# Kernel optimization log

Measured on AMD Instinct MI355X. Metric: run time of the kernel, lower is better.

The kernel has to match this reference:

```python
import jax, jax.numpy as jnp
import numpy as np

EPS = 1e-5

def layer_norm(x, gamma, beta):
    m = jnp.mean(x, axis=-1, keepdims=True)
    v = jnp.var(x, axis=-1, keepdims=True)
    return (x - m) / jnp.sqrt(v + EPS) * gamma + beta


def setup_inputs() -> dict:
    key = jax.random.key(0)
    ks = jax.random.split(key, 10)
    B, N, D = 2, 2048, 1024
    H, Dh = 16, 64
    C, CD = 256, 512
    inner = H * Dh  # 1024
    J = C + 1 + N  # 2305 = context + null + self

    x = jax.random.normal(ks[0], (B, N, D), dtype=jnp.float32)
    context = jax.random.normal(ks[1], (B, C, CD), dtype=jnp.float32)
    mask = jax.random.uniform(ks[2], (B, C + N)) < 0.9  # bool, mostly True
    attn_bias = jax.random.normal(ks[3], (H, N, J), dtype=jnp.float32) * 0.02

    norm_gamma = jnp.ones((D,), dtype=jnp.float32)
    null_kv = jax.random.normal(ks[4], (2, Dh), dtype=jnp.float32)
    Wq = jax.random.normal(ks[5], (D, inner), dtype=jnp.float32) * (D ** -0.5)
    Wkv = jax.random.normal(ks[6], (D, 2 * Dh), dtype=jnp.float32) * (D ** -0.5)
    ctx_ln_w = jnp.ones((CD,), dtype=jnp.float32)
    ctx_ln_b = jnp.zeros((CD,), dtype=jnp.float32)
    Wctx = jax.random.normal(ks[7], (CD, 2 * Dh), dtype=jnp.float32) * (CD ** -0.5)
    bctx = jnp.zeros((2 * Dh,), dtype=jnp.float32)
    Wout = jax.random.normal(ks[8], (inner, D), dtype=jnp.float32) * (inner ** -0.5)
    out_gamma = jnp.ones((D,), dtype=jnp.float32)

    return {"x": x, "context": context, "mask": mask, "attn_bias": attn_bias,
            "norm_gamma": norm_gamma, "null_kv": null_kv, "Wq": Wq, "Wkv": Wkv,
            "ctx_ln_w": ctx_ln_w, "ctx_ln_b": ctx_ln_b, "Wctx": Wctx, "bctx": bctx,
            "Wout": Wout, "out_gamma": out_gamma}


def reference(x, context, mask, attn_bias, norm_gamma, null_kv, Wq, Wkv,
              ctx_ln_w, ctx_ln_b, Wctx, bctx, Wout, out_gamma):
    B, N, D = x.shape
    Dh = null_kv.shape[-1]
    H = Wq.shape[-1] // Dh
    scale = Dh ** -0.5

    xn = layer_norm(x, norm_gamma, 0.0)
    q = (xn @ Wq).reshape(B, N, H, Dh).transpose(0, 2, 1, 3) * scale  # b h n d
    k, v = jnp.split(xn @ Wkv, 2, axis=-1)  # b n d each (multi-query: shared across heads)

    # prepend learned null kv token
    nk = jnp.broadcast_to(null_kv[0], (B, 1, Dh))
    nv = jnp.broadcast_to(null_kv[1], (B, 1, Dh))
    k = jnp.concatenate([nk, k], axis=1)
    v = jnp.concatenate([nv, v], axis=1)

    # prepend projected context tokens
    cn = layer_norm(context, ctx_ln_w, ctx_ln_b)
    ck, cv = jnp.split(cn @ Wctx + bctx, 2, axis=-1)
    k = jnp.concatenate([ck, k], axis=1)  # b j d, j = C + 1 + N
    v = jnp.concatenate([cv, v], axis=1)

    sim = jnp.einsum('bhid,bjd->bhij', q, k) + attn_bias
    # pad mask with True for the null token (left), then broadcast over h, i
    m = jnp.pad(mask, ((0, 0), (1, 0)), constant_values=True)[:, None, None, :]
    max_neg = -jnp.finfo(sim.dtype).max
    sim = jnp.where(m, sim, max_neg)

    attn = jax.nn.softmax(sim.astype(jnp.float32), axis=-1)
    out = jnp.einsum('bhij,bjd->bhid', attn, v)  # b h n d
    out = out.transpose(0, 2, 1, 3).reshape(B, N, H * Dh)
    return layer_norm(out @ Wout, out_gamma, 0.0)
```

## Files before the change

### kernel.cpp

```cpp
#include <hip/hip_runtime.h>

constexpr int B  = 2;
constexpr int N  = 2048;
constexpr int H  = 16;
constexpr int C  = 256;
constexpr int J  = C + 1 + N;
constexpr int Jp = 2368;
constexpr int NT = Jp / 64;
constexpr float EPS = 1e-5f;
constexpr float LOG2E = 1.4426950408889634f;

typedef __bf16 bf16x8 __attribute__((ext_vector_type(8)));
typedef float  f32x4  __attribute__((ext_vector_type(4)));
typedef float  f32x16 __attribute__((ext_vector_type(16)));
typedef unsigned int uint4v __attribute__((ext_vector_type(4)));
typedef __attribute__((address_space(3))) unsigned int lds_u32;
typedef const __attribute__((address_space(1))) unsigned int glb_u32;

__device__ inline void load_lds16(const void* g, void* l) {
    __builtin_amdgcn_global_load_lds((glb_u32*)g, (lds_u32*)l, 16, 0, 0);
}
__device__ inline unsigned short f2bf(float f) {
    unsigned int u = __builtin_bit_cast(unsigned int, f);
    u += 0x7fffu + ((u >> 16) & 1u);
    return (unsigned short)(u >> 16);
}
__device__ inline unsigned int packbf2(float a, float b) {
    union { __bf16 h[2]; unsigned int u; } cv;
    cv.h[0] = (__bf16)a;
    cv.h[1] = (__bf16)b;
    return cv.u;
}
__device__ inline float fexp2(float x) {
    float r;
    asm("v_exp_f32 %0, %1" : "=v"(r) : "v"(x));
    return r;
}
__device__ inline f32x4 mfma16(bf16x8 a, bf16x8 b, f32x4 c) {
    return __builtin_amdgcn_mfma_f32_16x16x32_bf16(a, b, c, 0, 0, 0);
}
__device__ inline f32x16 mfma32(bf16x8 a, bf16x8 b, f32x16 c) {
    return __builtin_amdgcn_mfma_f32_32x32x16_bf16(a, b, c, 0, 0, 0);
}
__device__ inline f32x4 loadu4(const float* p) {
    f32x4 r;
    __builtin_memcpy(&r, p, 16);
    return r;
}

__global__ void mask_prep(const void* __restrict__ mraw, float* __restrict__ maskf) {
    __shared__ int bad_int, bad_f32;
    const int t = threadIdx.x;
    if (t == 0) { bad_int = 0; bad_f32 = 0; }
    __syncthreads();
    const unsigned int* w = (const unsigned int*)mraw;
    int li = 0, lf = 0;
    for (int i = t; i < 1152; i += 256) {
        unsigned int v = w[i];
        if (v > 1u) li = 1;
        if (v != 0u && v != 0x3F800000u) lf = 1;
    }
    if (li) atomicOr(&bad_int, 1);
    if (lf) atomicOr(&bad_f32, 1);
    __syncthreads();
    const int mode = (!bad_int) ? 0 : ((!bad_f32) ? 1 : 2);
    const unsigned char* bytes = (const unsigned char*)mraw;
    for (int i = t; i < 2 * Jp; i += 256) {
        const int b2 = i / Jp, jp = i - b2 * Jp;
        float v;
        if (jp == 0) v = 0.f;
        else if (jp >= J) v = -1e30f;
        else {
            const int idx = b2 * (C + N) + jp - 1;
            const int keep = (mode == 2) ? (bytes[idx] != 0) : (w[idx] != 0u);
            v = keep ? 0.f : -1e30f;
        }
        maskf[i] = v;
    }
}

__global__ void zero_pads(unsigned short* __restrict__ Kb, unsigned short* __restrict__ Vt) {
    const int t = threadIdx.x;
    for (int i = t; i < 2 * 63 * 64; i += 256) {
        const int b2 = i / (63 * 64);
        const int rr = (i / 64) % 63;
        const int d  = i % 64;
        Kb[(size_t)(b2 * Jp + J + rr) * 64 + d] = 0;
    }
    for (int i = t; i < 2 * 64 * 63; i += 256) {
        const int b2 = i / (64 * 63);
        const int d  = (i / 63) % 64;
        const int cc = i % 63;
        Vt[(size_t)(b2 * 64 + d) * Jp + J + cc] = 0;
    }
}

template <int BF16OUT>
__global__ void __launch_bounds__(256) ln1024(const float* __restrict__ x,
                                              const float* __restrict__ gamma,
                                              void* __restrict__ outp) {
    const int row = blockIdx.x;
    const int t = threadIdx.x;
    const float* xr = x + (size_t)row * 1024;
    float4 v = ((const float4*)xr)[t];
    float s  = v.x + v.y + v.z + v.w;
    float ss = v.x * v.x + v.y * v.y + v.z * v.z + v.w * v.w;
    #pragma unroll
    for (int o = 1; o < 64; o <<= 1) {
        s  += __shfl_xor(s, o);
        ss += __shfl_xor(ss, o);
    }
    __shared__ float red[8];
    const int w = t >> 6;
    if ((t & 63) == 0) { red[w * 2] = s; red[w * 2 + 1] = ss; }
    __syncthreads();
    s  = red[0] + red[2] + red[4] + red[6];
    ss = red[1] + red[3] + red[5] + red[7];
    const float mean = s * (1.0f / 1024.0f);
    const float var  = ss * (1.0f / 1024.0f) - mean * mean;
    const float rstd = rsqrtf(var + EPS);
    const float4 g = ((const float4*)gamma)[t];
    float o0 = (v.x - mean) * rstd * g.x;
    float o1 = (v.y - mean) * rstd * g.y;
    float o2 = (v.z - mean) * rstd * g.z;
    float o3 = (v.w - mean) * rstd * g.w;
    if (BF16OUT) {
        ushort4 u;
        u.x = f2bf(o0); u.y = f2bf(o1); u.z = f2bf(o2); u.w = f2bf(o3);
        *(ushort4*)((unsigned short*)outp + (size_t)row * 1024 + t * 4) = u;
    } else {
        *(float4*)((float*)outp + (size_t)row * 1024 + t * 4) = make_float4(o0, o1, o2, o3);
    }
}

__global__ void __launch_bounds__(256) transpose_w(const float* __restrict__ W,
                                                   unsigned short* __restrict__ WT,
                                                   int K, int Nn, float scale) {
    __shared__ float lds[64][68];
    const int k0 = blockIdx.x * 64, n0 = blockIdx.y * 64;
    const int t = threadIdx.x;
    const int kk = t >> 4, nn = (t & 15) * 4;
    #pragma unroll
    for (int r = 0; r < 4; r++) {
        const float4 v = *(const float4*)(W + (size_t)(k0 + kk + r * 16) * Nn + n0 + nn);
        lds[kk + r * 16][nn + 0] = v.x;
        lds[kk + r * 16][nn + 1] = v.y;
        lds[kk + r * 16][nn + 2] = v.z;
        lds[kk + r * 16][nn + 3] = v.w;
    }
    __syncthreads();
    const int nr = t >> 2, kc = (t & 3) * 16;
    #pragma unroll
    for (int u4 = 0; u4 < 4; u4++) {
        ushort4 u;
        u.x = f2bf(lds[kc + u4 * 4 + 0][nr] * scale);
        u.y = f2bf(lds[kc + u4 * 4 + 1][nr] * scale);
        u.z = f2bf(lds[kc + u4 * 4 + 2][nr] * scale);
        u.w = f2bf(lds[kc + u4 * 4 + 3][nr] * scale);
        *(ushort4*)(WT + (size_t)(n0 + nr) * K + k0 + kc + u4 * 4) = u;
    }
}

__global__ void __launch_bounds__(128) ctx_proj(const float* __restrict__ ctx,
                                                const float* __restrict__ lw,
                                                const float* __restrict__ lb,
                                                const float* __restrict__ Wc,
                                                const float* __restrict__ bc,
                                                unsigned short* __restrict__ Kb,
                                                unsigned short* __restrict__ Vt) {
    const int row = blockIdx.x;
    const int b2 = row >> 8, ci = row & 255;
    const int t = threadIdx.x;
    __shared__ float cn[512];
    __shared__ float red[4];
    const float* xr = ctx + (size_t)row * 512;
    float4 v = ((const float4*)xr)[t];
    float s  = v.x + v.y + v.z + v.w;
    float ss = v.x * v.x + v.y * v.y + v.z * v.z + v.w * v.w;
    #pragma unroll
    for (int o = 1; o < 64; o <<= 1) {
        s  += __shfl_xor(s, o);
        ss += __shfl_xor(ss, o);
    }
    const int w = t >> 6;
    if ((t & 63) == 0) { red[w * 2] = s; red[w * 2 + 1] = ss; }
    __syncthreads();
    s  = red[0] + red[2];
    ss = red[1] + red[3];
    const float mean = s * (1.0f / 512.0f);
    const float var  = ss * (1.0f / 512.0f) - mean * mean;
    const float rstd = rsqrtf(var + EPS);
    const float4 g  = ((const float4*)lw)[t];
    const float4 be = ((const float4*)lb)[t];
    float4 c4;
    c4.x = (v.x - mean) * rstd * g.x + be.x;
    c4.y = (v.y - mean) * rstd * g.y + be.y;
    c4.z = (v.z - mean) * rstd * g.z + be.z;
    c4.w = (v.w - mean) * rstd * g.w + be.w;
    *(float4*)&cn[t * 4] = c4;
    __syncthreads();
    float acc = bc[t];
    #pragma unroll 8
    for (int d = 0; d < 512; d++) acc = fmaf(cn[d], Wc[d * 128 + t], acc);
    const unsigned short bv = f2bf(acc);
    if (t < 64) Kb[(size_t)(b2 * Jp + ci) * 64 + t] = bv;
    else        Vt[(size_t)(b2 * 64 + (t - 64)) * Jp + ci] = bv;
}

__global__ void null_fill(const float* __restrict__ nkv,
                          unsigned short* __restrict__ Kb, unsigned short* __restrict__ Vt) {
    const int b2 = blockIdx.x;
    const int t = threadIdx.x;
    Kb[(size_t)(b2 * Jp + 256) * 64 + t] = f2bf(nkv[t]);
    Vt[(size_t)(b2 * 64 + t) * Jp + 256] = f2bf(nkv[64 + t]);
}

template <int MODE>
__global__ void __launch_bounds__(256, 2) gemm_bf16(
        const unsigned short* __restrict__ A, const unsigned short* __restrict__ BT,
        float* __restrict__ Cf, unsigned short* __restrict__ Cb,
        unsigned short* __restrict__ Kb, unsigned short* __restrict__ Vt,
        int M, int Nn, int K) {
    __shared__ __align__(16) unsigned char smem[65536];
    const int t = threadIdx.x;
    const int w = t >> 6, lane = t & 63;
    const int g = lane >> 4, ln15 = lane & 15;
    const int wm = w >> 1, wn = w & 1;
    const int row0 = blockIdx.x * 128, col0 = blockIdx.y * 128;
    const int nk = K >> 6;
    const int ls = lane >> 3;
    const int swz = (lane & 7) ^ ls;

    f32x4 acc[4][4];
    #pragma unroll
    for (int i = 0; i < 4; i++)
        #pragma unroll
        for (int jj = 0; jj < 4; jj++)
            acc[i][jj] = (f32x4){0.f, 0.f, 0.f, 0.f};

    auto stage = [&](int kt, int cur) {
        if (w < 2) {
            const unsigned short* src = A + (size_t)(row0 + w * 64 + ls) * K + kt * 64 + swz * 8;
            unsigned char* dst = smem + cur * 16384 + w * 8192;
            #pragma unroll
            for (int i = 0; i < 8; i++)
                load_lds16(src + (size_t)i * 8 * K, dst + i * 1024);
        } else {
            const unsigned short* src = BT + (size_t)(col0 + (w - 2) * 64 + ls) * K + kt * 64 + swz * 8;
            unsigned char* dst = smem + 32768 + cur * 16384 + (w - 2) * 8192;
            #pragma unroll
            for (int i = 0; i < 8; i++)
                load_lds16(src + (size_t)i * 8 * K, dst + i * 1024);
        }
    };

    stage(0, 0);
    __syncthreads();
    for (int kt = 0; kt < nk; kt++) {
        const int cur = kt & 1;
        if (kt + 1 < nk) stage(kt + 1, cur ^ 1);
        const unsigned char* As = smem + cur * 16384;
        const unsigned char* Bs = smem + 32768 + cur * 16384;
        #pragma unroll
        for (int ks = 0; ks < 2; ks++) {
            bf16x8 af[4], bf[4];
            #pragma unroll
            for (int mq = 0; mq < 4; mq++)
                af[mq] = *(const bf16x8*)(As + (wm * 64 + mq * 16 + ln15) * 128 +
                                          ((ks * 64 + g * 16) ^ ((ln15 & 7) << 4)));
            #pragma unroll
            for (int nq = 0; nq < 4; nq++)
                bf[nq] = *(const bf16x8*)(Bs + (wn * 64 + nq * 16 + ln15) * 128 +
                                          ((ks * 64 + g * 16) ^ ((ln15 & 7) << 4)));
            #pragma unroll
            for (int mq = 0; mq < 4; mq++)
                #pragma unroll
                for (int nq = 0; nq < 4; nq++)
                    acc[mq][nq] = mfma16(af[mq], bf[nq], acc[mq][nq]);
        }
        __syncthreads();
    }

    #pragma unroll
    for (int mq = 0; mq < 4; mq++) {
        #pragma unroll
        for (int nq = 0; nq < 4; nq++) {
            #pragma unroll
            for (int r = 0; r < 4; r++) {
                const int gr = row0 + wm * 64 + mq * 16 + g * 4 + r;
                const int gc = col0 + wn * 64 + nq * 16 + ln15;
                if (MODE == 0) {
                    Cf[(size_t)gr * Nn + gc] = acc[mq][nq][r];
                } else if (MODE == 1) {
                    Cb[(size_t)gr * Nn + gc] = f2bf(acc[mq][nq][r]);
                } else {
                    const int b2 = gr >> 11, tok = gr & 2047;
                    const unsigned short v = f2bf(acc[mq][nq][r]);
                    if (gc < 64) Kb[(size_t)(b2 * Jp + 257 + tok) * 64 + gc] = v;
                    else         Vt[(size_t)(b2 * 64 + gc - 64) * Jp + 257 + tok] = v;
                }
            }
        }
    }
}

__global__ void __launch_bounds__(512, 2) attn_v11(
        const unsigned short* __restrict__ qb, const unsigned short* __restrict__ Kb,
        const unsigned short* __restrict__ Vt, const float* __restrict__ bias,
        const float* __restrict__ maskf, unsigned short* __restrict__ aout) {
    __shared__ __align__(16) unsigned char smem[143360];
    const int t = threadIdx.x;
    const int w = t >> 6, lane = t & 63;
    const int l31 = lane & 31, hi = lane >> 5;
    const int i0 = blockIdx.x * 128, h = blockIdx.y;
    const int b2 = w & 1, wq = w >> 1;
    const int ls = lane >> 3;
    const int swz = (lane & 7) ^ ls;
    const int rsw = (lane & 7) << 4;

    auto stage = [&](int jt, int cur) {
        const int j0 = jt * 64;
        const int half = w & 1;
        if (w < 4) {
            const int kb = w >> 1;
            const unsigned short* src = Kb + (size_t)(kb * Jp + j0 + half * 32 + ls) * 64 + swz * 8;
            unsigned char* dst = smem + cur * 32768 + kb * 8192 + half * 4096;
            #pragma unroll
            for (int i = 0; i < 4; i++)
                load_lds16(src + (size_t)i * 8 * 64, dst + i * 1024);
        } else {
            const int vb = (w - 4) >> 1;
            const unsigned short* src = Vt + (size_t)(vb * 64 + half * 32 + ls) * Jp + j0 + swz * 8;
            unsigned char* dst = smem + cur * 32768 + 16384 + vb * 8192 + half * 4096;
            #pragma unroll
            for (int i = 0; i < 4; i++)
                load_lds16(src + (size_t)i * 8 * Jp, dst + i * 1024);
        }
    };

    const int bq = t >> 2;
    const int bs = (t & 3) * 16;
    const float* biasQrow = bias + ((size_t)h * N + i0 + bq) * J;
    auto bias_issue = [&](int jt, f32x4& r0, f32x4& r1, f32x4& r2, f32x4& r3) {
        const int j0 = jt * 64;
        if (j0 + 64 <= J) {
            r0 = loadu4(biasQrow + j0 + bs + 0);
            r1 = loadu4(biasQrow + j0 + bs + 4);
            r2 = loadu4(biasQrow + j0 + bs + 8);
            r3 = loadu4(biasQrow + j0 + bs + 12);
        } else {
            #pragma unroll
            for (int c = 0; c < 4; c++) {
                const int ja = j0 + bs + c;
                r0[c] = (ja      < J) ? biasQrow[ja]      : 0.f;
                r1[c] = (ja + 4  < J) ? biasQrow[ja + 4]  : 0.f;
                r2[c] = (ja + 8  < J) ? biasQrow[ja + 8]  : 0.f;
                r3[c] = (ja + 12 < J) ? biasQrow[ja + 12] : 0.f;
            }
        }
    };
    auto bias_write = [&](int cur, const f32x4& r0, const f32x4& r1,
                          const f32x4& r2, const f32x4& r3) {
        float* basep = (float*)(smem + 65536 + cur * 38912) + bq * 76 + bs;
        *(f32x4*)(basep + 0)  = r0;
        *(f32x4*)(basep + 4)  = r1;
        *(f32x4*)(basep + 8)  = r2;
        *(f32x4*)(basep + 12) = r3;
    };

    bf16x8 qf[4];
    #pragma unroll
    for (int ks = 0; ks < 4; ks++)
        qf[ks] = *(const bf16x8*)(qb + (size_t)(b2 * N + i0 + wq * 32 + l31) * 1024 +
                                  h * 64 + ks * 16 + hi * 8);

    float mrun = -1e30f, lrun = 0.f;
    f32x16 outA[2];
    outA[0] = (f32x16)0.f;
    outA[1] = (f32x16)0.f;

    auto compute = [&](int jt, int cur) {
        const int j0 = jt * 64;
        const unsigned char* Kl = smem + cur * 32768 + b2 * 8192;
        const unsigned char* Vl = smem + cur * 32768 + 16384 + b2 * 8192;
        const float* bbL = (const float*)(smem + 65536 + cur * 38912) +
                           (wq * 32 + l31) * 76;

        f32x16 S[2];
        S[0] = (f32x16)0.f;
        S[1] = (f32x16)0.f;
        #pragma unroll
        for (int jh = 0; jh < 2; jh++) {
            const int krow = jh * 32 + l31;
            bf16x8 ka[4];
            #pragma unroll
            for (int ks = 0; ks < 4; ks++)
                ka[ks] = *(const bf16x8*)(Kl + krow * 128 + ((ks * 32 + hi * 16) ^ rsw));
            __builtin_amdgcn_s_setprio(1);
            #pragma unroll
            for (int ks = 0; ks < 4; ks++)
                S[jh] = mfma32(ka[ks], qf[ks], S[jh]);
            __builtin_amdgcn_s_setprio(0);
        }

        float sv[2][16];
        #pragma unroll
        for (int jh = 0; jh < 2; jh++)
            #pragma unroll
            for (int rg = 0; rg < 4; rg++) {
                const f32x4 br = *(const f32x4*)(bbL + jh * 32 + rg * 8 + hi * 4);
                const f32x4 mk = *(const f32x4*)(maskf + b2 * Jp + j0 + jh * 32 + rg * 8 + hi * 4);
                #pragma unroll
                for (int c = 0; c < 4; c++)
                    sv[jh][rg * 4 + c] = fmaf(br[c], LOG2E, S[jh][rg * 4 + c]) + mk[c];
            }

        float tm = sv[0][0];
        #pragma unroll
        for (int jh = 0; jh < 2; jh++)
            #pragma unroll
            for (int r = 0; r < 16; r++)
                tm = fmaxf(tm, sv[jh][r]);
        tm = fmaxf(tm, __shfl_xor(tm, 32));

        if (!__all(tm <= mrun)) {
            const float mnew = fmaxf(mrun, tm);
            const float cor = fexp2(mrun - mnew);
            mrun = mnew;
            #pragma unroll
            for (int i = 0; i < 16; i++) { outA[0][i] *= cor; outA[1][i] *= cor; }
            lrun *= cor;
        }
        const float mcur = mrun;

        float p[2][16];
        float ts = 0.f;
        #pragma unroll
        for (int jh = 0; jh < 2; jh++)
            #pragma unroll
            for (int r = 0; r < 16; r++) {
                p[jh][r] = fexp2(sv[jh][r] - mcur);
                ts += p[jh][r];
            }
        ts += __shfl_xor(ts, 32);
        lrun += ts;

        #pragma unroll
        for (int jh = 0; jh < 2; jh++) {
            #pragma unroll
            for (int m = 0; m < 2; m++) {
                const unsigned int a0 = packbf2(p[jh][m * 8 + 0], p[jh][m * 8 + 1]);
                const unsigned int a1 = packbf2(p[jh][m * 8 + 2], p[jh][m * 8 + 3]);
                const unsigned int b0 = packbf2(p[jh][m * 8 + 4], p[jh][m * 8 + 5]);
                const unsigned int b1 = packbf2(p[jh][m * 8 + 6], p[jh][m * 8 + 7]);
                const unsigned int xa0 = (unsigned int)__shfl_xor((int)a0, 32);
                const unsigned int xa1 = (unsigned int)__shfl_xor((int)a1, 32);
                const unsigned int xb0 = (unsigned int)__shfl_xor((int)b0, 32);
                const unsigned int xb1 = (unsigned int)__shfl_xor((int)b1, 32);
                uint4v wd;
                wd[0] = hi ? xb0 : a0;
                wd[1] = hi ? xb1 : a1;
                wd[2] = hi ? b0 : xa0;
                wd[3] = hi ? b1 : xa1;
                const bf16x8 pfrag = __builtin_bit_cast(bf16x8, wd);
                bf16x8 va[2];
                #pragma unroll
                for (int dblk = 0; dblk < 2; dblk++)
                    va[dblk] = *(const bf16x8*)(Vl + (dblk * 32 + l31) * 128 +
                               ((jh * 64 + m * 32 + hi * 16) ^ rsw));
                __builtin_amdgcn_s_setprio(1);
                #pragma unroll
                for (int dblk = 0; dblk < 2; dblk++)
                    outA[dblk] = mfma32(va[dblk], pfrag, outA[dblk]);
                __builtin_amdgcn_s_setprio(0);
            }
        }
    };

    f32x4 bR0, bR1, bR2, bR3;
    bias_issue(0, bR0, bR1, bR2, bR3);
    stage(0, 0);
    bias_write(0, bR0, bR1, bR2, bR3);
    __syncthreads();
    for (int jt = 0; jt < NT; jt++) {
        const int cur = jt & 1;
        if (jt + 1 < NT) {
            bias_issue(jt + 1, bR0, bR1, bR2, bR3);
            stage(jt + 1, cur ^ 1);
        }
        compute(jt, cur);
        if (jt + 1 < NT) bias_write(cur ^ 1, bR0, bR1, bR2, bR3);
        __syncthreads();
    }

    const float inv = 1.0f / lrun;
    unsigned short* orow = aout + (size_t)(b2 * N + i0 + wq * 32 + l31) * 1024 + h * 64;
    #pragma unroll
    for (int dblk = 0; dblk < 2; dblk++)
        #pragma unroll
        for (int rg = 0; rg < 4; rg++)
            #pragma unroll
            for (int c2 = 0; c2 < 2; c2++) {
                const int r = rg * 4 + c2 * 2;
                const unsigned int u = packbf2(outA[dblk][r] * inv, outA[dblk][r + 1] * inv);
                *(unsigned int*)(orow + dblk * 32 + rg * 8 + hi * 4 + c2 * 2) = u;
            }
}

extern "C" void kernel_launch(void* const* d_in, const int* in_sizes, int n_in,
                              void* d_out, int out_size, void* d_ws, size_t ws_size,
                              hipStream_t stream) {
    const float* x         = (const float*)d_in[0];
    const float* context   = (const float*)d_in[1];
    const void*  mask      = d_in[2];
    const float* bias      = (const float*)d_in[3];
    const float* norm_g    = (const float*)d_in[4];
    const float* null_kv   = (const float*)d_in[5];
    const float* Wq        = (const float*)d_in[6];
    const float* Wkv       = (const float*)d_in[7];
    const float* ctx_ln_w  = (const float*)d_in[8];
    const float* ctx_ln_b  = (const float*)d_in[9];
    const float* Wctx      = (const float*)d_in[10];
    const float* bctx      = (const float*)d_in[11];
    const float* Wout      = (const float*)d_in[12];
    const float* out_gamma = (const float*)d_in[13];
    float* out = (float*)d_out;

    unsigned char* wsb = (unsigned char*)d_ws;
    unsigned short* xnb   = (unsigned short*)(wsb + 0);
    unsigned short* qbb   = (unsigned short*)(wsb + 8388608);
    float*          y     = (float*)(wsb + 0);
    unsigned short* aoutp = (unsigned short*)(wsb + 16777216);
    unsigned short* KbP   = (unsigned short*)(wsb + 25165824);
    unsigned short* VtP   = (unsigned short*)(wsb + 25772032);
    float*          maskf = (float*)(wsb + 26378240);
    unsigned short* WqT   = (unsigned short*)(wsb + 26397184);
    unsigned short* WkvT  = (unsigned short*)(wsb + 28494336);
    unsigned short* WoutT = (unsigned short*)(wsb + 28756480);

    mask_prep<<<1, 256, 0, stream>>>(mask, maskf);
    zero_pads<<<1, 256, 0, stream>>>(KbP, VtP);
    ln1024<1><<<B * N, 256, 0, stream>>>(x, norm_g, xnb);
    transpose_w<<<dim3(16, 16), 256, 0, stream>>>(Wq, WqT, 1024, 1024, 0.125f * LOG2E);
    transpose_w<<<dim3(16, 2), 256, 0, stream>>>(Wkv, WkvT, 1024, 128, 1.0f);
    transpose_w<<<dim3(16, 16), 256, 0, stream>>>(Wout, WoutT, 1024, 1024, 1.0f);
    ctx_proj<<<B * C, 128, 0, stream>>>(context, ctx_ln_w, ctx_ln_b, Wctx, bctx, KbP, VtP);
    null_fill<<<B, 64, 0, stream>>>(null_kv, KbP, VtP);
    gemm_bf16<1><<<dim3(32, 8), 256, 0, stream>>>(xnb, WqT, nullptr, qbb, nullptr, nullptr, 4096, 1024, 1024);
    gemm_bf16<2><<<dim3(32, 1), 256, 0, stream>>>(xnb, WkvT, nullptr, nullptr, KbP, VtP, 4096, 128, 1024);
    attn_v11<<<dim3(16, 16), 512, 0, stream>>>(qbb, KbP, VtP, bias, maskf, aoutp);
    gemm_bf16<0><<<dim3(32, 8), 256, 0, stream>>>(aoutp, WoutT, y, nullptr, nullptr, nullptr, 4096, 1024, 1024);
    ln1024<0><<<B * N, 256, 0, stream>>>(y, out_gamma, out);
}
```

Measured before the change: 254.0 us.

## Split attention along key axis into two segments and merge partials with LSE combine

The attention kernel now runs a third grid dimension that splits the key tiles into two segments. Each block writes a normalized bf16 partial output and a log-sum-exp value, and a new combine kernel merges the two partials. Shared memory drops from double-buffered to single-buffered (71.7KB), so up to four blocks can be resident instead of two, and the grid grows from 256 to 512 blocks for better CU fill on the MI355X. The cost is that tile loads no longer overlap compute, plus an extra kernel launch and round trips to global memory for the partials. Storing partials in bf16 also adds some rounding error.

Measured after the change: 284.0 us. 1.12x slower.

```diff
diff --git a/kernel.cpp b/kernel.cpp
--- a/kernel.cpp
+++ b/kernel.cpp
@@ -30,6 +30,9 @@
     cv.h[0] = (__bf16)a;
     cv.h[1] = (__bf16)b;
     return cv.u;
+}
+__device__ inline float bf2f(unsigned short u) {
+    return __builtin_bit_cast(float, (unsigned int)u << 16);
 }
 __device__ inline float fexp2(float x) {
     float r;
@@ -304,34 +307,39 @@
     }
 }
 
-__global__ void __launch_bounds__(512, 2) attn_v11(
+__global__ void __launch_bounds__(512, 4) attn_v12(
         const unsigned short* __restrict__ qb, const unsigned short* __restrict__ Kb,
         const unsigned short* __restrict__ Vt, const float* __restrict__ bias,
-        const float* __restrict__ maskf, unsigned short* __restrict__ aout) {
-    __shared__ __align__(16) unsigned char smem[143360];
+        const float* __restrict__ maskf,
+        unsigned short* __restrict__ opartA, unsigned short* __restrict__ opartB,
+        float* __restrict__ lsebuf) {
+    __shared__ __align__(16) unsigned char smem[71680];
     const int t = threadIdx.x;
     const int w = t >> 6, lane = t & 63;
     const int l31 = lane & 31, hi = lane >> 5;
     const int i0 = blockIdx.x * 128, h = blockIdx.y;
+    const int jseg = blockIdx.z;
+    const int jt_beg = jseg * 19;
+    const int jt_end = jseg ? NT : 19;
     const int b2 = w & 1, wq = w >> 1;
     const int ls = lane >> 3;
     const int swz = (lane & 7) ^ ls;
     const int rsw = (lane & 7) << 4;
 
-    auto stage = [&](int jt, int cur) {
+    auto stage = [&](int jt) {
         const int j0 = jt * 64;
         const int half = w & 1;
         if (w < 4) {
             const int kb = w >> 1;
             const unsigned short* src = Kb + (size_t)(kb * Jp + j0 + half * 32 + ls) * 64 + swz * 8;
-            unsigned char* dst = smem + cur * 32768 + kb * 8192 + half * 4096;
+            unsigned char* dst = smem + kb * 8192 + half * 4096;
             #pragma unroll
             for (int i = 0; i < 4; i++)
                 load_lds16(src + (size_t)i * 8 * 64, dst + i * 1024);
         } else {
             const int vb = (w - 4) >> 1;
             const unsigned short* src = Vt + (size_t)(vb * 64 + half * 32 + ls) * Jp + j0 + swz * 8;
-            unsigned char* dst = smem + cur * 32768 + 16384 + vb * 8192 + half * 4096;
+            unsigned char* dst = smem + 16384 + vb * 8192 + half * 4096;
             #pragma unroll
             for (int i = 0; i < 4; i++)
                 load_lds16(src + (size_t)i * 8 * Jp, dst + i * 1024);
@@ -359,9 +367,9 @@
             }
         }
     };
-    auto bias_write = [&](int cur, const f32x4& r0, const f32x4& r1,
+    auto bias_write = [&](const f32x4& r0, const f32x4& r1,
                           const f32x4& r2, const f32x4& r3) {
-        float* basep = (float*)(smem + 65536 + cur * 38912) + bq * 76 + bs;
+        float* basep = (float*)(smem + 32768) + bq * 76 + bs;
         *(f32x4*)(basep + 0)  = r0;
         *(f32x4*)(basep + 4)  = r1;
         *(f32x4*)(basep + 8)  = r2;
@@ -379,12 +387,11 @@
     outA[0] = (f32x16)0.f;
     outA[1] = (f32x16)0.f;
 
-    auto compute = [&](int jt, int cur) {
+    auto compute = [&](int jt) {
         const int j0 = jt * 64;
-        const unsigned char* Kl = smem + cur * 32768 + b2 * 8192;
-        const unsigned char* Vl = smem + cur * 32768 + 16384 + b2 * 8192;
-        const float* bbL = (const float*)(smem + 65536 + cur * 38912) +
-                           (wq * 32 + l31) * 76;
+        const unsigned char* Kl = smem + b2 * 8192;
+        const unsigned char* Vl = smem + 16384 + b2 * 8192;
+        const float* bbL = (const float*)(smem + 32768) + (wq * 32 + l31) * 76;
 
         f32x16 S[2];
         S[0] = (f32x16)0.f;
@@ -478,23 +485,19 @@
     };
 
     f32x4 bR0, bR1, bR2, bR3;
-    bias_issue(0, bR0, bR1, bR2, bR3);
-    stage(0, 0);
-    bias_write(0, bR0, bR1, bR2, bR3);
-    __syncthreads();
-    for (int jt = 0; jt < NT; jt++) {
-        const int cur = jt & 1;
-        if (jt + 1 < NT) {
-            bias_issue(jt + 1, bR0, bR1, bR2, bR3);
-            stage(jt + 1, cur ^ 1);
-        }
-        compute(jt, cur);
-        if (jt + 1 < NT) bias_write(cur ^ 1, bR0, bR1, bR2, bR3);
+    bias_issue(jt_beg, bR0, bR1, bR2, bR3);
+    for (int jt = jt_beg; jt < jt_end; jt++) {
+        stage(jt);
+        bias_write(bR0, bR1, bR2, bR3);
         __syncthreads();
+        if (jt + 1 < jt_end) bias_issue(jt + 1, bR0, bR1, bR2, bR3);
+        compute(jt);
+        __syncthreads();
     }
 
     const float inv = 1.0f / lrun;
-    unsigned short* orow = aout + (size_t)(b2 * N + i0 + wq * 32 + l31) * 1024 + h * 64;
+    unsigned short* opart = jseg ? opartB : opartA;
+    unsigned short* orow = opart + (size_t)(b2 * N + i0 + wq * 32 + l31) * 1024 + h * 64;
     #pragma unroll
     for (int dblk = 0; dblk < 2; dblk++)
         #pragma unroll
@@ -505,6 +508,32 @@
                 const unsigned int u = packbf2(outA[dblk][r] * inv, outA[dblk][r + 1] * inv);
                 *(unsigned int*)(orow + dblk * 32 + rg * 8 + hi * 4 + c2 * 2) = u;
             }
+    if (hi == 0)
+        lsebuf[(size_t)jseg * 65536 + (size_t)(b2 * N + i0 + wq * 32 + l31) * 16 + h] =
+            mrun + __log2f(lrun);
+}
+
+__global__ void __launch_bounds__(256) combine(const unsigned short* __restrict__ opartA,
+                                               unsigned short* __restrict__ opartBio,
+                                               const float* __restrict__ lsebuf) {
+    const int row = blockIdx.x;
+    const int c = threadIdx.x * 4;
+    const int h = c >> 6;
+    const float lA = lsebuf[(size_t)row * 16 + h];
+    const float lB = lsebuf[65536 + (size_t)row * 16 + h];
+    const float M = fmaxf(lA, lB);
+    float wA = fexp2(lA - M), wB = fexp2(lB - M);
+    const float inv = 1.0f / (wA + wB);
+    wA *= inv; wB *= inv;
+    const size_t base = (size_t)row * 1024 + c;
+    const ushort4 a4 = *(const ushort4*)(opartA + base);
+    const ushort4 b4 = *(const ushort4*)(opartBio + base);
+    ushort4 o4;
+    o4.x = f2bf(wA * bf2f(a4.x) + wB * bf2f(b4.x));
+    o4.y = f2bf(wA * bf2f(a4.y) + wB * bf2f(b4.y));
+    o4.z = f2bf(wA * bf2f(a4.z) + wB * bf2f(b4.z));
+    o4.w = f2bf(wA * bf2f(a4.w) + wB * bf2f(b4.w));
+    *(ushort4*)(opartBio + base) = o4;
 }
 
 extern "C" void kernel_launch(void* const* d_in, const int* in_sizes, int n_in,
@@ -531,12 +560,14 @@
     unsigned short* qbb   = (unsigned short*)(wsb + 8388608);
     float*          y     = (float*)(wsb + 0);
     unsigned short* aoutp = (unsigned short*)(wsb + 16777216);
+    unsigned short* opartA = xnb;
     unsigned short* KbP   = (unsigned short*)(wsb + 25165824);
     unsigned short* VtP   = (unsigned short*)(wsb + 25772032);
     float*          maskf = (float*)(wsb + 26378240);
     unsigned short* WqT   = (unsigned short*)(wsb + 26397184);
     unsigned short* WkvT  = (unsigned short*)(wsb + 28494336);
     unsigned short* WoutT = (unsigned short*)(wsb + 28756480);
+    float*          lsebuf = (float*)(wsb + 30853632);
 
     mask_prep<<<1, 256, 0, stream>>>(mask, maskf);
     zero_pads<<<1, 256, 0, stream>>>(KbP, VtP);
@@ -548,7 +579,9 @@
     null_fill<<<B, 64, 0, stream>>>(null_kv, KbP, VtP);
     gemm_bf16<1><<<dim3(32, 8), 256, 0, stream>>>(xnb, WqT, nullptr, qbb, nullptr, nullptr, 4096, 1024, 1024);
     gemm_bf16<2><<<dim3(32, 1), 256, 0, stream>>>(xnb, WkvT, nullptr, nullptr, KbP, VtP, 4096, 128, 1024);
-    attn_v11<<<dim3(16, 16), 512, 0, stream>>>(qbb, KbP, VtP, bias, maskf, aoutp);
+    attn_v12<<<dim3(16, 16, 2), 512, 0, stream>>>(qbb, KbP, VtP, bias, maskf,
+                                                  opartA, aoutp, lsebuf);
+    combine<<<dim3(B * N), 256, 0, stream>>>(opartA, aoutp, lsebuf);
     gemm_bf16<0><<<dim3(32, 8), 256, 0, stream>>>(aoutp, WoutT, y, nullptr, nullptr, nullptr, 4096, 1024, 1024);
     ln1024<0><<<B * N, 256, 0, stream>>>(y, out_gamma, out);
 }
```
